# Optimization experiments

Measured on AMD Instinct MI355X. Metric: run time of the kernel, lower is better.

The kernel has to match this reference:

```python
import jax, jax.numpy as jnp
import numpy as np


def setup_inputs() -> dict:
    key = jax.random.key(0)
    k1, k2, k3 = jax.random.split(key, 3)
    N, L, S, H, D = 2, 2048, 2048, 8, 64
    return {
        "queries": jax.random.normal(k1, (N, L, H, D), dtype=jnp.float32),
        "keys": jax.random.normal(k2, (N, S, H, D), dtype=jnp.float32),
        "values": jax.random.normal(k3, (N, S, H, D), dtype=jnp.float32),
        "q_mask": jnp.ones((N, L), dtype=bool),
        "kv_mask": jnp.ones((N, S), dtype=bool),
    }


def reference(queries, keys, values, q_mask, kv_mask):
    # QK^T: [N, L, S, H]
    qk = jnp.einsum("nlhd,nshd->nlsh", queries, keys)
    # mask: True where attention is allowed
    mask = q_mask[:, :, None, None] & kv_mask[:, None, :, None]
    qk = jnp.where(mask, qk, -jnp.inf)
    softmax_temp = 1.0 / np.sqrt(queries.shape[3]).astype(np.float32)
    A = jax.nn.softmax(softmax_temp * qk, axis=2)  # over S
    out = jnp.einsum("nlsh,nshd->nlhd", A, values)
    return out
```

## Files before the change

### kernel.cpp

```cpp
#include <hip/hip_runtime.h>
#include <hip/hip_bf16.h>

#define N_B 2
#define L_Q 2048
#define S_K 2048
#define N_H 8
#define D_H 64
#define HD  512
#define KVB 64
#define NT  (S_K / KVB)
#define RS  72
#define LOG2E 1.4426950408889634f

typedef __attribute__((ext_vector_type(8))) short bf16x8;
typedef __attribute__((ext_vector_type(4))) short short4v;
typedef __attribute__((ext_vector_type(4))) float f32x4;

__device__ __forceinline__ short f2bf(float f) {
  union { float f; unsigned u; } v; v.f = f;
  return (short)((v.u + 0x7FFFu + ((v.u >> 16) & 1u)) >> 16);
}
__device__ __forceinline__ float bf2f(short s) {
  union { unsigned u; float f; } w; w.u = ((unsigned)(unsigned short)s) << 16;
  return w.f;
}
__device__ __forceinline__ bf16x8 pack8(float4 a, float4 b) {
  bf16x8 t;
  t[0]=f2bf(a.x); t[1]=f2bf(a.y); t[2]=f2bf(a.z); t[3]=f2bf(a.w);
  t[4]=f2bf(b.x); t[5]=f2bf(b.y); t[6]=f2bf(b.z); t[7]=f2bf(b.w);
  return t;
}

__global__ __launch_bounds__(256)
void preconv_kernel(const float* __restrict__ K, const float* __restrict__ V,
                    const int* __restrict__ kvm,
                    short* __restrict__ kws, short* __restrict__ vws,
                    unsigned long long* __restrict__ mws) {
  const size_t i = (size_t)blockIdx.x * 256 + threadIdx.x;
  const float4* kp = (const float4*)K + i * 2;
  float4 a = kp[0], b = kp[1];
  *(bf16x8*)(kws + i * 8) = pack8(a, b);
  const float4* vp = (const float4*)V + i * 2;
  float4 c = vp[0], d = vp[1];
  *(bf16x8*)(vws + i * 8) = pack8(c, d);
  if (blockIdx.x == 0 && threadIdx.x < (N_B * S_K / 64)) {
    const int* src = kvm + threadIdx.x * 64;
    unsigned long long m = 0;
    #pragma unroll 8
    for (int bb = 0; bb < 64; ++bb) m |= (src[bb] ? 1ull : 0ull) << bb;
    mws[threadIdx.x] = m;
  }
}

__global__ __launch_bounds__(128, 2)
void attn_fwd_v2(const float* __restrict__ Q, const short* __restrict__ Kb,
                 const short* __restrict__ Vb,
                 const unsigned long long* __restrict__ mbits,
                 float* __restrict__ Out) {
  __shared__ __align__(128) short kt[2 * 4096];
  __shared__ __align__(128) short vt[2 * 4096];
  __shared__ __align__(16)  short pl[2][16 * RS];

  const int tid  = threadIdx.x;
  const int wid  = tid >> 6;
  const int lane = tid & 63;
  const int l16  = lane & 15;
  const int lg   = lane >> 4;

  const int logical = ((blockIdx.x & 7) << 7) | (blockIdx.x >> 3);
  const int nh = logical >> 6;
  const int qb = logical & 63;
  const int n  = nh >> 3;
  const int h  = nh & 7;
  const int q0 = qb * 32 + wid * 16;

  const float* Qn = Q  + ((size_t)n * L_Q) * HD + h * D_H;
  const char*  Kn = (const char*)(Kb + ((size_t)n * S_K) * HD + h * D_H);
  const char*  Vn = (const char*)(Vb + ((size_t)n * S_K) * HD + h * D_H);

  int koffb[4], voffb[4];
  #pragma unroll
  for (int i = 0; i < 4; ++i) {
    const int p   = wid * 4096 + i * 1024 + lane * 16;
    const int row = p >> 7;
    const int cb  = (p & 127) ^ ((row & 7) << 4);
    koffb[i] = row * 1024 + cb;
    const int k  = ((p >> 9) << 2) | ((p >> 5) & 3);
    const int d  = (((p >> 7) & 3) << 4) | ((p >> 1) & 15);
    voffb[i] = k * 1024 + d * 2;
  }

  bf16x8 qf[2];
  {
    const float* qp = Qn + (size_t)(q0 + l16) * HD + lg * 8;
    #pragma unroll
    for (int c = 0; c < 2; ++c) {
      float4 a = *(const float4*)(qp + c * 32);
      float4 b = *(const float4*)(qp + c * 32 + 4);
      float4 as, bs;
      as.x=a.x*0.125f; as.y=a.y*0.125f; as.z=a.z*0.125f; as.w=a.w*0.125f;
      bs.x=b.x*0.125f; bs.y=b.y*0.125f; bs.z=b.z*0.125f; bs.w=b.w*0.125f;
      qf[c] = pack8(as, bs);
    }
  }

  const int swz    = (l16 & 7) << 4;
  const int kaddrA = l16 * 128 + ((lg * 16) ^ swz);
  const int kaddrB = l16 * 128 + ((64 + lg * 16) ^ swz);
  const int vlane  = lg * 1024 + l16 * 8;
  const unsigned kt0 = (unsigned)(size_t)(__attribute__((address_space(3))) char*)((char*)&kt[0]);
  const unsigned vt0 = (unsigned)(size_t)(__attribute__((address_space(3))) char*)((char*)&vt[0]);

  f32x4 o[4];
  #pragma unroll
  for (int g = 0; g < 4; ++g) o[g] = (f32x4){0.f, 0.f, 0.f, 0.f};
  float m_run[4], l_run[4];
  #pragma unroll
  for (int r = 0; r < 4; ++r) { m_run[r] = -3e38f; l_run[r] = 0.f; }

  short* pw = pl[wid];

  #define ISSUE(t_) do {                                                          \
    const int bs_ = ((t_) & 1) * 8192;                                            \
    const char* ks_ = Kn + (size_t)(t_) * 65536;                                  \
    const char* vs_ = Vn + (size_t)(t_) * 65536;                                  \
    _Pragma("unroll")                                                             \
    for (int i_ = 0; i_ < 4; ++i_) {                                              \
      __builtin_amdgcn_global_load_lds(                                           \
        (const __attribute__((address_space(1))) void*)(ks_ + koffb[i_]),         \
        (__attribute__((address_space(3))) void*)((char*)kt + bs_ + wid*4096 + i_*1024), \
        16, 0, 0);                                                                \
      __builtin_amdgcn_global_load_lds(                                           \
        (const __attribute__((address_space(1))) void*)(vs_ + voffb[i_]),         \
        (__attribute__((address_space(3))) void*)((char*)vt + bs_ + wid*4096 + i_*1024), \
        16, 0, 0);                                                                \
    }                                                                             \
  } while (0)

  ISSUE(0);

  for (int t = 0; t < NT; ++t) {
    __syncthreads();
    if (t + 1 < NT) ISSUE(t + 1);
    const int bo = (t & 1) * 8192;

    f32x4 sc[4];
    #pragma unroll
    for (int g = 0; g < 4; ++g) {
      bf16x8 kb0 = *(const bf16x8*)((const char*)kt + bo + g * 2048 + kaddrA);
      bf16x8 kb1 = *(const bf16x8*)((const char*)kt + bo + g * 2048 + kaddrB);
      f32x4 z = (f32x4){0.f, 0.f, 0.f, 0.f};
      z = __builtin_amdgcn_mfma_f32_16x16x32_bf16(qf[0], kb0, z, 0, 0, 0);
      z = __builtin_amdgcn_mfma_f32_16x16x32_bf16(qf[1], kb1, z, 0, 0, 0);
      sc[g] = z;
    }

    const unsigned long long mb = mbits[n * NT + t];
    #pragma unroll
    for (int g = 0; g < 4; ++g) {
      if (!((mb >> (g * 16 + l16)) & 1ull)) {
        #pragma unroll
        for (int r = 0; r < 4; ++r) sc[g][r] = -3e38f;
      }
    }

    float mt[4];
    #pragma unroll
    for (int r = 0; r < 4; ++r) {
      float v = fmaxf(fmaxf(sc[0][r], sc[1][r]), fmaxf(sc[2][r], sc[3][r]));
      v = fmaxf(v, __shfl_xor(v, 1));
      v = fmaxf(v, __shfl_xor(v, 2));
      v = fmaxf(v, __shfl_xor(v, 4));
      v = fmaxf(v, __shfl_xor(v, 8));
      mt[r] = v;
    }
    float alpha[4];
    #pragma unroll
    for (int r = 0; r < 4; ++r) {
      float mn = fmaxf(m_run[r], mt[r]);
      alpha[r] = __builtin_amdgcn_exp2f((m_run[r] - mn) * LOG2E);
      m_run[r] = mn;
    }
    float rsum[4] = {0.f, 0.f, 0.f, 0.f};
    short pb[4][4];
    #pragma unroll
    for (int g = 0; g < 4; ++g) {
      #pragma unroll
      for (int r = 0; r < 4; ++r) {
        float p = __builtin_amdgcn_exp2f((sc[g][r] - m_run[r]) * LOG2E);
        short s = f2bf(p);
        pb[g][r] = s;
        rsum[r] += bf2f(s);
      }
    }
    #pragma unroll
    for (int r = 0; r < 4; ++r) {
      float v = rsum[r];
      v += __shfl_xor(v, 1);
      v += __shfl_xor(v, 2);
      v += __shfl_xor(v, 4);
      v += __shfl_xor(v, 8);
      l_run[r] = l_run[r] * alpha[r] + v;
    }
    #pragma unroll
    for (int g = 0; g < 4; ++g) {
      f32x4 tv = o[g];
      #pragma unroll
      for (int r = 0; r < 4; ++r) tv[r] *= alpha[r];
      o[g] = tv;
    }

    #pragma unroll
    for (int g = 0; g < 4; ++g)
      #pragma unroll
      for (int r = 0; r < 4; ++r)
        pw[(lg * 4 + r) * RS + g * 16 + l16] = pb[g][r];

    bf16x8 pa0 = *(const bf16x8*)&pw[l16 * RS + lg * 8];
    bf16x8 pa1 = *(const bf16x8*)&pw[l16 * RS + 32 + lg * 8];

    const unsigned va = vt0 + (unsigned)(bo + vlane);
    #define TRRD(dst, off) asm volatile("ds_read_b64_tr_b16 %0, %1 offset:" off \
                                        : "=v"(dst) : "v"(va))
    short4v w0la, w0lb, w0ha, w0hb, w1la, w1lb, w1ha, w1hb;
    short4v w2la, w2lb, w2ha, w2hb, w3la, w3lb, w3ha, w3hb;
    TRRD(w0la, "0");   TRRD(w0lb, "512"); TRRD(w0ha, "4096"); TRRD(w0hb, "4608");
    TRRD(w1la, "128"); TRRD(w1lb, "640"); TRRD(w1ha, "4224"); TRRD(w1hb, "4736");
    TRRD(w2la, "256"); TRRD(w2lb, "768"); TRRD(w2ha, "4352"); TRRD(w2hb, "4864");
    TRRD(w3la, "384"); TRRD(w3lb, "896"); TRRD(w3ha, "4480"); TRRD(w3hb, "4992");
    asm volatile("s_waitcnt lgkmcnt(0)" ::: "memory");
    __builtin_amdgcn_sched_barrier(0);

    bf16x8 v0l = __builtin_shufflevector(w0la, w0lb, 0,1,2,3,4,5,6,7);
    bf16x8 v0h = __builtin_shufflevector(w0ha, w0hb, 0,1,2,3,4,5,6,7);
    bf16x8 v1l = __builtin_shufflevector(w1la, w1lb, 0,1,2,3,4,5,6,7);
    bf16x8 v1h = __builtin_shufflevector(w1ha, w1hb, 0,1,2,3,4,5,6,7);
    bf16x8 v2l = __builtin_shufflevector(w2la, w2lb, 0,1,2,3,4,5,6,7);
    bf16x8 v2h = __builtin_shufflevector(w2ha, w2hb, 0,1,2,3,4,5,6,7);
    bf16x8 v3l = __builtin_shufflevector(w3la, w3lb, 0,1,2,3,4,5,6,7);
    bf16x8 v3h = __builtin_shufflevector(w3ha, w3hb, 0,1,2,3,4,5,6,7);

    o[0] = __builtin_amdgcn_mfma_f32_16x16x32_bf16(pa0, v0l, o[0], 0, 0, 0);
    o[0] = __builtin_amdgcn_mfma_f32_16x16x32_bf16(pa1, v0h, o[0], 0, 0, 0);
    o[1] = __builtin_amdgcn_mfma_f32_16x16x32_bf16(pa0, v1l, o[1], 0, 0, 0);
    o[1] = __builtin_amdgcn_mfma_f32_16x16x32_bf16(pa1, v1h, o[1], 0, 0, 0);
    o[2] = __builtin_amdgcn_mfma_f32_16x16x32_bf16(pa0, v2l, o[2], 0, 0, 0);
    o[2] = __builtin_amdgcn_mfma_f32_16x16x32_bf16(pa1, v2h, o[2], 0, 0, 0);
    o[3] = __builtin_amdgcn_mfma_f32_16x16x32_bf16(pa0, v3l, o[3], 0, 0, 0);
    o[3] = __builtin_amdgcn_mfma_f32_16x16x32_bf16(pa1, v3h, o[3], 0, 0, 0);
  }

  float* op = Out + ((size_t)n * L_Q + q0) * HD + h * D_H;
  float inv[4];
  #pragma unroll
  for (int r = 0; r < 4; ++r) inv[r] = 1.0f / l_run[r];
  #pragma unroll
  for (int gd = 0; gd < 4; ++gd)
    #pragma unroll
    for (int r = 0; r < 4; ++r)
      op[(size_t)(lg * 4 + r) * HD + gd * 16 + l16] = o[gd][r] * inv[r];
}

__global__ __launch_bounds__(256, 2)
void attn_fwd_kernel(const float* __restrict__ Q, const float* __restrict__ K,
                     const float* __restrict__ V,
                     const int* __restrict__ q_mask,
                     const int* __restrict__ kv_mask,
                     float* __restrict__ Out) {
  __shared__ __align__(16) short kts[KVB * RS];
  __shared__ __align__(16) short vts[D_H * RS];
  __shared__ __align__(16) short pls[4][16 * RS];
  const int tid = threadIdx.x, wid = tid >> 6, lane = tid & 63;
  const int l16 = lane & 15, lg = lane >> 4;
  const int bid = blockIdx.x, nh = bid >> 5, qb = bid & 31;
  const int n = nh >> 3, h = nh & 7, q0 = qb * 64 + wid * 16;
  const float* Qb = Q + ((size_t)n * L_Q) * HD + h * D_H;
  const float* Kb = K + ((size_t)n * S_K) * HD + h * D_H;
  const float* Vb = V + ((size_t)n * S_K) * HD + h * D_H;
  const int* km = kv_mask + (size_t)n * S_K;
  (void)q_mask;
  bf16x8 qf[2];
  {
    const float* qp = Qb + (size_t)(q0 + l16) * HD + lg * 8;
    #pragma unroll
    for (int c = 0; c < 2; ++c) {
      float4 a = *(const float4*)(qp + c * 32);
      float4 b = *(const float4*)(qp + c * 32 + 4);
      float4 as, bs;
      as.x=a.x*0.125f; as.y=a.y*0.125f; as.z=a.z*0.125f; as.w=a.w*0.125f;
      bs.x=b.x*0.125f; bs.y=b.y*0.125f; bs.z=b.z*0.125f; bs.w=b.w*0.125f;
      qf[c] = pack8(as, bs);
    }
  }
  f32x4 o[4];
  #pragma unroll
  for (int g = 0; g < 4; ++g) o[g] = (f32x4){0.f, 0.f, 0.f, 0.f};
  float m_run[4], l_run[4];
  #pragma unroll
  for (int r = 0; r < 4; ++r) { m_run[r] = -3e38f; l_run[r] = 0.f; }
  for (int s0 = 0; s0 < S_K; s0 += KVB) {
    __syncthreads();
    {
      const int cid = tid << 1, row = cid >> 3, c0 = cid & 7;
      const float* kp = Kb + (size_t)(s0 + row) * HD + c0 * 8;
      float4 f0 = *(const float4*)(kp), f1 = *(const float4*)(kp + 4);
      float4 f2 = *(const float4*)(kp + 8), f3 = *(const float4*)(kp + 12);
      *(bf16x8*)&kts[row * RS + c0 * 8]     = pack8(f0, f1);
      *(bf16x8*)&kts[row * RS + c0 * 8 + 8] = pack8(f2, f3);
    }
    {
      const int kv = tid >> 2, dc = tid & 3;
      const float* vp = Vb + (size_t)(s0 + kv) * HD + dc * 16;
      float4 f0 = *(const float4*)(vp), f1 = *(const float4*)(vp + 4);
      float4 f2 = *(const float4*)(vp + 8), f3 = *(const float4*)(vp + 12);
      float tv[16] = { f0.x,f0.y,f0.z,f0.w, f1.x,f1.y,f1.z,f1.w,
                       f2.x,f2.y,f2.z,f2.w, f3.x,f3.y,f3.z,f3.w };
      short* dst = &vts[(dc * 16) * RS + kv];
      #pragma unroll
      for (int j = 0; j < 16; ++j) dst[j * RS] = f2bf(tv[j]);
    }
    __syncthreads();
    f32x4 sc[4];
    #pragma unroll
    for (int g = 0; g < 4; ++g) {
      bf16x8 kb0 = *(const bf16x8*)&kts[(g*16 + l16) * RS + lg * 8];
      bf16x8 kb1 = *(const bf16x8*)&kts[(g*16 + l16) * RS + 32 + lg * 8];
      f32x4 z = (f32x4){0.f, 0.f, 0.f, 0.f};
      z = __builtin_amdgcn_mfma_f32_16x16x32_bf16(qf[0], kb0, z, 0, 0, 0);
      z = __builtin_amdgcn_mfma_f32_16x16x32_bf16(qf[1], kb1, z, 0, 0, 0);
      sc[g] = z;
    }
    #pragma unroll
    for (int g = 0; g < 4; ++g) {
      float b = km[s0 + g*16 + l16] ? 0.f : -3e38f;
      #pragma unroll
      for (int r = 0; r < 4; ++r) sc[g][r] += b;
    }
    float mt[4];
    #pragma unroll
    for (int r = 0; r < 4; ++r) {
      float v = fmaxf(fmaxf(sc[0][r], sc[1][r]), fmaxf(sc[2][r], sc[3][r]));
      v = fmaxf(v, __shfl_xor(v, 1)); v = fmaxf(v, __shfl_xor(v, 2));
      v = fmaxf(v, __shfl_xor(v, 4)); v = fmaxf(v, __shfl_xor(v, 8));
      mt[r] = v;
    }
    float alpha[4];
    #pragma unroll
    for (int r = 0; r < 4; ++r) {
      float mn = fmaxf(m_run[r], mt[r]);
      alpha[r] = __builtin_amdgcn_exp2f((m_run[r] - mn) * LOG2E);
      m_run[r] = mn;
    }
    float rsum[4] = {0.f, 0.f, 0.f, 0.f};
    short pb[4][4];
    #pragma unroll
    for (int g = 0; g < 4; ++g)
      #pragma unroll
      for (int r = 0; r < 4; ++r) {
        float p = __builtin_amdgcn_exp2f((sc[g][r] - m_run[r]) * LOG2E);
        short s = f2bf(p); pb[g][r] = s; rsum[r] += bf2f(s);
      }
    #pragma unroll
    for (int r = 0; r < 4; ++r) {
      float v = rsum[r];
      v += __shfl_xor(v, 1); v += __shfl_xor(v, 2);
      v += __shfl_xor(v, 4); v += __shfl_xor(v, 8);
      l_run[r] = l_run[r] * alpha[r] + v;
    }
    #pragma unroll
    for (int g = 0; g < 4; ++g)
      #pragma unroll
      for (int r = 0; r < 4; ++r) o[g][r] *= alpha[r];
    short* pwf = pls[wid];
    #pragma unroll
    for (int g = 0; g < 4; ++g)
      #pragma unroll
      for (int r = 0; r < 4; ++r)
        pwf[(lg*4 + r) * RS + g*16 + l16] = pb[g][r];
    __syncthreads();
    bf16x8 pa0 = *(const bf16x8*)&pwf[l16 * RS + lg * 8];
    bf16x8 pa1 = *(const bf16x8*)&pwf[l16 * RS + 32 + lg * 8];
    #pragma unroll
    for (int gd = 0; gd < 4; ++gd) {
      bf16x8 vb0 = *(const bf16x8*)&vts[(gd*16 + l16) * RS + lg * 8];
      bf16x8 vb1 = *(const bf16x8*)&vts[(gd*16 + l16) * RS + 32 + lg * 8];
      o[gd] = __builtin_amdgcn_mfma_f32_16x16x32_bf16(pa0, vb0, o[gd], 0, 0, 0);
      o[gd] = __builtin_amdgcn_mfma_f32_16x16x32_bf16(pa1, vb1, o[gd], 0, 0, 0);
    }
  }
  float* op = Out + ((size_t)n * L_Q + q0) * HD + h * D_H;
  float inv[4];
  #pragma unroll
  for (int r = 0; r < 4; ++r) inv[r] = 1.0f / l_run[r];
  #pragma unroll
  for (int gd = 0; gd < 4; ++gd)
    #pragma unroll
    for (int r = 0; r < 4; ++r)
      op[(size_t)(lg*4 + r) * HD + gd*16 + l16] = o[gd][r] * inv[r];
}

extern "C" void kernel_launch(void* const* d_in, const int* in_sizes, int n_in,
                              void* d_out, int out_size, void* d_ws, size_t ws_size,
                              hipStream_t stream) {
  const float* Q = (const float*)d_in[0];
  const float* K = (const float*)d_in[1];
  const float* V = (const float*)d_in[2];
  const int* qm = (const int*)d_in[3];
  const int* km = (const int*)d_in[4];
  float* Out = (float*)d_out;
  (void)in_sizes; (void)n_in; (void)out_size;

  const size_t kbytes = (size_t)N_B * S_K * HD * 2;
  const size_t need = 2 * kbytes + 512;
  if (ws_size >= need) {
    short* kws = (short*)d_ws;
    short* vws = (short*)((char*)d_ws + kbytes);
    unsigned long long* mws = (unsigned long long*)((char*)d_ws + 2 * kbytes);
    hipLaunchKernelGGL(preconv_kernel, dim3(1024), dim3(256), 0, stream,
                       K, V, km, kws, vws, mws);
    hipLaunchKernelGGL(attn_fwd_v2, dim3(1024), dim3(128), 0, stream,
                       Q, kws, vws, mws, Out);
  } else {
    hipLaunchKernelGGL(attn_fwd_kernel, dim3(512), dim3(256), 0, stream,
                       Q, K, V, qm, km, Out);
  }
}
```

Baseline: 147.0 us.

## Rewrite attention with 32x32 MFMA, split-KV, transposed V, and lazy rescale

```diff
diff --git a/kernel.cpp b/kernel.cpp
--- a/kernel.cpp
+++ b/kernel.cpp
@@ -8,13 +8,18 @@
 #define D_H 64
 #define HD  512
 #define KVB 64
-#define NT  (S_K / KVB)
+#define NT  32
+#define NSP 3
 #define RS  72
+#define PQT ((size_t)N_B * L_Q * N_H)
 #define LOG2E 1.4426950408889634f
-
-typedef __attribute__((ext_vector_type(8))) short bf16x8;
-typedef __attribute__((ext_vector_type(4))) short short4v;
-typedef __attribute__((ext_vector_type(4))) float f32x4;
+#define DEFER_THR 11.5f
+
+typedef __attribute__((ext_vector_type(8)))  short bf16x8;
+typedef __attribute__((ext_vector_type(4)))  short short4v;
+typedef __attribute__((ext_vector_type(4)))  float f32x4;
+typedef __attribute__((ext_vector_type(16))) float f32x16;
+typedef __attribute__((ext_vector_type(4)))  unsigned int u32x4;
 
 __device__ __forceinline__ short f2bf(float f) {
   union { float f; unsigned u; } v; v.f = f;
@@ -30,19 +35,35 @@
   t[4]=f2bf(b.x); t[5]=f2bf(b.y); t[6]=f2bf(b.z); t[7]=f2bf(b.w);
   return t;
 }
+__device__ __forceinline__ unsigned cvtpk(float a, float b) {
+  unsigned d;
+  asm("v_cvt_pk_bf16_f32 %0, %1, %2" : "=v"(d) : "v"(a), "v"(b));
+  return d;
+}
 
 __global__ __launch_bounds__(256)
 void preconv_kernel(const float* __restrict__ K, const float* __restrict__ V,
                     const int* __restrict__ kvm,
-                    short* __restrict__ kws, short* __restrict__ vws,
+                    short* __restrict__ kws, short* __restrict__ vtws,
                     unsigned long long* __restrict__ mws) {
   const size_t i = (size_t)blockIdx.x * 256 + threadIdx.x;
   const float4* kp = (const float4*)K + i * 2;
   float4 a = kp[0], b = kp[1];
   *(bf16x8*)(kws + i * 8) = pack8(a, b);
-  const float4* vp = (const float4*)V + i * 2;
-  float4 c = vp[0], d = vp[1];
-  *(bf16x8*)(vws + i * 8) = pack8(c, d);
+  {
+    const size_t e0 = i * 8;
+    const float4* vp = (const float4*)(V + e0);
+    float4 c = vp[0], d = vp[1];
+    const int n   = (int)(e0 >> 20);
+    const int rem = (int)(e0 & 1048575u);
+    const int kv  = rem >> 9;
+    const int hd  = rem & 511;
+    const int h   = hd >> 6, d0 = hd & 63;
+    short* dst = vtws + ((size_t)((n * 8 + h) * 64 + d0)) * 2048 + kv;
+    float tv[8] = { c.x,c.y,c.z,c.w, d.x,d.y,d.z,d.w };
+    #pragma unroll
+    for (int j = 0; j < 8; ++j) dst[(size_t)j * 2048] = f2bf(tv[j]);
+  }
   if (blockIdx.x == 0 && threadIdx.x < (N_B * S_K / 64)) {
     const int* src = kvm + threadIdx.x * 64;
     unsigned long long m = 0;
@@ -52,213 +73,198 @@
   }
 }
 
-__global__ __launch_bounds__(128, 2)
-void attn_fwd_v2(const float* __restrict__ Q, const short* __restrict__ Kb,
-                 const short* __restrict__ Vb,
-                 const unsigned long long* __restrict__ mbits,
-                 float* __restrict__ Out) {
+__global__ __launch_bounds__(256, 3)
+void attn_fwd32(const float* __restrict__ Q, const short* __restrict__ Kb,
+                const short* __restrict__ Vtb,
+                const unsigned long long* __restrict__ mbits,
+                short* __restrict__ Owb, float* __restrict__ Mw,
+                float* __restrict__ Lw) {
   __shared__ __align__(128) short kt[2 * 4096];
   __shared__ __align__(128) short vt[2 * 4096];
-  __shared__ __align__(16)  short pl[2][16 * RS];
 
   const int tid  = threadIdx.x;
   const int wid  = tid >> 6;
   const int lane = tid & 63;
-  const int l16  = lane & 15;
-  const int lg   = lane >> 4;
-
-  const int logical = ((blockIdx.x & 7) << 7) | (blockIdx.x >> 3);
-  const int nh = logical >> 6;
-  const int qb = logical & 63;
-  const int n  = nh >> 3;
-  const int h  = nh & 7;
-  const int q0 = qb * 32 + wid * 16;
-
-  const float* Qn = Q  + ((size_t)n * L_Q) * HD + h * D_H;
-  const char*  Kn = (const char*)(Kb + ((size_t)n * S_K) * HD + h * D_H);
-  const char*  Vn = (const char*)(Vb + ((size_t)n * S_K) * HD + h * D_H);
-
-  int koffb[4], voffb[4];
-  #pragma unroll
-  for (int i = 0; i < 4; ++i) {
-    const int p   = wid * 4096 + i * 1024 + lane * 16;
+  const int l31  = lane & 31;
+  const int hi   = lane >> 5;
+
+  const int logical = (blockIdx.x & 7) * 96 + (blockIdx.x >> 3);
+  const int qb   = logical & 15;
+  const int rest = logical >> 4;
+  const int sp   = rest % NSP;
+  const int nh   = rest / NSP;
+  const int n = nh >> 3;
+  const int h = nh & 7;
+  const int q0 = qb * 128 + wid * 32;
+  const int t0 = sp * 11;
+  const int t1 = (sp == 2) ? NT : (t0 + 11);
+
+  const float* Qn  = Q + ((size_t)n * L_Q) * HD + h * D_H;
+  const char*  Kn  = (const char*)(Kb + ((size_t)n * S_K) * HD + h * D_H);
+  const char*  Vtn = (const char*)(Vtb + ((size_t)(n * 8 + h) * 64) * 2048);
+
+  int koffb[2], voffb[2];
+  #pragma unroll
+  for (int i = 0; i < 2; ++i) {
+    const int p   = tid * 16 + i * 4096;
     const int row = p >> 7;
-    const int cb  = (p & 127) ^ ((row & 7) << 4);
-    koffb[i] = row * 1024 + cb;
-    const int k  = ((p >> 9) << 2) | ((p >> 5) & 3);
-    const int d  = (((p >> 7) & 3) << 4) | ((p >> 1) & 15);
-    voffb[i] = k * 1024 + d * 2;
-  }
-
-  bf16x8 qf[2];
+    const int g   = (p & 127) ^ ((row & 7) << 4);
+    koffb[i] = row * 1024 + g;
+    voffb[i] = row * 4096 + g;
+  }
+
+  bf16x8 qf[4];
   {
-    const float* qp = Qn + (size_t)(q0 + l16) * HD + lg * 8;
-    #pragma unroll
-    for (int c = 0; c < 2; ++c) {
-      float4 a = *(const float4*)(qp + c * 32);
-      float4 b = *(const float4*)(qp + c * 32 + 4);
+    const float sq = 0.125f * LOG2E;
+    const float* qp = Qn + (size_t)(q0 + l31) * HD + hi * 8;
+    #pragma unroll
+    for (int dc = 0; dc < 4; ++dc) {
+      float4 a = *(const float4*)(qp + dc * 16);
+      float4 b = *(const float4*)(qp + dc * 16 + 4);
       float4 as, bs;
-      as.x=a.x*0.125f; as.y=a.y*0.125f; as.z=a.z*0.125f; as.w=a.w*0.125f;
-      bs.x=b.x*0.125f; bs.y=b.y*0.125f; bs.z=b.z*0.125f; bs.w=b.w*0.125f;
-      qf[c] = pack8(as, bs);
-    }
-  }
-
-  const int swz    = (l16 & 7) << 4;
-  const int kaddrA = l16 * 128 + ((lg * 16) ^ swz);
-  const int kaddrB = l16 * 128 + ((64 + lg * 16) ^ swz);
-  const int vlane  = lg * 1024 + l16 * 8;
-  const unsigned kt0 = (unsigned)(size_t)(__attribute__((address_space(3))) char*)((char*)&kt[0]);
-  const unsigned vt0 = (unsigned)(size_t)(__attribute__((address_space(3))) char*)((char*)&vt[0]);
-
-  f32x4 o[4];
-  #pragma unroll
-  for (int g = 0; g < 4; ++g) o[g] = (f32x4){0.f, 0.f, 0.f, 0.f};
-  float m_run[4], l_run[4];
-  #pragma unroll
-  for (int r = 0; r < 4; ++r) { m_run[r] = -3e38f; l_run[r] = 0.f; }
-
-  short* pw = pl[wid];
+      as.x=a.x*sq; as.y=a.y*sq; as.z=a.z*sq; as.w=a.w*sq;
+      bs.x=b.x*sq; bs.y=b.y*sq; bs.z=b.z*sq; bs.w=b.w*sq;
+      qf[dc] = pack8(as, bs);
+    }
+  }
+
+  const int swz = (l31 & 7) << 4;
+  f32x16 o0 = {}, o1 = {};
+  float m = 0.f, ls = 0.f;
 
   #define ISSUE(t_) do {                                                          \
     const int bs_ = ((t_) & 1) * 8192;                                            \
     const char* ks_ = Kn + (size_t)(t_) * 65536;                                  \
-    const char* vs_ = Vn + (size_t)(t_) * 65536;                                  \
+    const char* vs_ = Vtn + (size_t)(t_) * 128;                                   \
     _Pragma("unroll")                                                             \
-    for (int i_ = 0; i_ < 4; ++i_) {                                              \
+    for (int i_ = 0; i_ < 2; ++i_) {                                              \
       __builtin_amdgcn_global_load_lds(                                           \
         (const __attribute__((address_space(1))) void*)(ks_ + koffb[i_]),         \
-        (__attribute__((address_space(3))) void*)((char*)kt + bs_ + wid*4096 + i_*1024), \
+        (__attribute__((address_space(3))) void*)((char*)kt + bs_ + wid*1024 + i_*4096), \
         16, 0, 0);                                                                \
       __builtin_amdgcn_global_load_lds(                                           \
         (const __attribute__((address_space(1))) void*)(vs_ + voffb[i_]),         \
-        (__attribute__((address_space(3))) void*)((char*)vt + bs_ + wid*4096 + i_*1024), \
+        (__attribute__((address_space(3))) void*)((char*)vt + bs_ + wid*1024 + i_*4096), \
         16, 0, 0);                                                                \
     }                                                                             \
   } while (0)
 
-  ISSUE(0);
-
-  for (int t = 0; t < NT; ++t) {
+  ISSUE(t0);
+
+  for (int t = t0; t < t1; ++t) {
     __syncthreads();
-    if (t + 1 < NT) ISSUE(t + 1);
+    if (t + 1 < t1) ISSUE(t + 1);
     const int bo = (t & 1) * 8192;
 
-    f32x4 sc[4];
-    #pragma unroll
-    for (int g = 0; g < 4; ++g) {
-      bf16x8 kb0 = *(const bf16x8*)((const char*)kt + bo + g * 2048 + kaddrA);
-      bf16x8 kb1 = *(const bf16x8*)((const char*)kt + bo + g * 2048 + kaddrB);
-      f32x4 z = (f32x4){0.f, 0.f, 0.f, 0.f};
-      z = __builtin_amdgcn_mfma_f32_16x16x32_bf16(qf[0], kb0, z, 0, 0, 0);
-      z = __builtin_amdgcn_mfma_f32_16x16x32_bf16(qf[1], kb1, z, 0, 0, 0);
-      sc[g] = z;
+    f32x16 a0 = {}, a1 = {};
+    #pragma unroll
+    for (int dc = 0; dc < 4; ++dc) {
+      const int co = (dc * 32 + hi * 16) ^ swz;
+      bf16x8 kf0 = *(const bf16x8*)((const char*)kt + bo + l31 * 128 + co);
+      bf16x8 kf1 = *(const bf16x8*)((const char*)kt + bo + (32 + l31) * 128 + co);
+      a0 = __builtin_amdgcn_mfma_f32_32x32x16_bf16(kf0, qf[dc], a0, 0, 0, 0);
+      a1 = __builtin_amdgcn_mfma_f32_32x32x16_bf16(kf1, qf[dc], a1, 0, 0, 0);
     }
 
     const unsigned long long mb = mbits[n * NT + t];
-    #pragma unroll
-    for (int g = 0; g < 4; ++g) {
-      if (!((mb >> (g * 16 + l16)) & 1ull)) {
-        #pragma unroll
-        for (int r = 0; r < 4; ++r) sc[g][r] = -3e38f;
+    if (mb != ~0ull) {
+      #pragma unroll
+      for (int r = 0; r < 16; ++r) {
+        const int kv0 = (r & 3) + 8 * (r >> 2) + 4 * hi;
+        if (!((mb >> kv0) & 1ull))        a0[r] = -3e38f;
+        if (!((mb >> (kv0 + 32)) & 1ull)) a1[r] = -3e38f;
       }
     }
 
-    float mt[4];
-    #pragma unroll
-    for (int r = 0; r < 4; ++r) {
-      float v = fmaxf(fmaxf(sc[0][r], sc[1][r]), fmaxf(sc[2][r], sc[3][r]));
-      v = fmaxf(v, __shfl_xor(v, 1));
-      v = fmaxf(v, __shfl_xor(v, 2));
-      v = fmaxf(v, __shfl_xor(v, 4));
-      v = fmaxf(v, __shfl_xor(v, 8));
-      mt[r] = v;
-    }
-    float alpha[4];
-    #pragma unroll
-    for (int r = 0; r < 4; ++r) {
-      float mn = fmaxf(m_run[r], mt[r]);
-      alpha[r] = __builtin_amdgcn_exp2f((m_run[r] - mn) * LOG2E);
-      m_run[r] = mn;
-    }
-    float rsum[4] = {0.f, 0.f, 0.f, 0.f};
-    short pb[4][4];
-    #pragma unroll
-    for (int g = 0; g < 4; ++g) {
-      #pragma unroll
-      for (int r = 0; r < 4; ++r) {
-        float p = __builtin_amdgcn_exp2f((sc[g][r] - m_run[r]) * LOG2E);
-        short s = f2bf(p);
-        pb[g][r] = s;
-        rsum[r] += bf2f(s);
-      }
-    }
-    #pragma unroll
-    for (int r = 0; r < 4; ++r) {
-      float v = rsum[r];
-      v += __shfl_xor(v, 1);
-      v += __shfl_xor(v, 2);
-      v += __shfl_xor(v, 4);
-      v += __shfl_xor(v, 8);
-      l_run[r] = l_run[r] * alpha[r] + v;
-    }
-    #pragma unroll
-    for (int g = 0; g < 4; ++g) {
-      f32x4 tv = o[g];
-      #pragma unroll
-      for (int r = 0; r < 4; ++r) tv[r] *= alpha[r];
-      o[g] = tv;
-    }
-
-    #pragma unroll
-    for (int g = 0; g < 4; ++g)
-      #pragma unroll
-      for (int r = 0; r < 4; ++r)
-        pw[(lg * 4 + r) * RS + g * 16 + l16] = pb[g][r];
-
-    bf16x8 pa0 = *(const bf16x8*)&pw[l16 * RS + lg * 8];
-    bf16x8 pa1 = *(const bf16x8*)&pw[l16 * RS + 32 + lg * 8];
-
-    const unsigned va = vt0 + (unsigned)(bo + vlane);
-    #define TRRD(dst, off) asm volatile("ds_read_b64_tr_b16 %0, %1 offset:" off \
-                                        : "=v"(dst) : "v"(va))
-    short4v w0la, w0lb, w0ha, w0hb, w1la, w1lb, w1ha, w1hb;
-    short4v w2la, w2lb, w2ha, w2hb, w3la, w3lb, w3ha, w3hb;
-    TRRD(w0la, "0");   TRRD(w0lb, "512"); TRRD(w0ha, "4096"); TRRD(w0hb, "4608");
-    TRRD(w1la, "128"); TRRD(w1lb, "640"); TRRD(w1ha, "4224"); TRRD(w1hb, "4736");
-    TRRD(w2la, "256"); TRRD(w2lb, "768"); TRRD(w2ha, "4352"); TRRD(w2hb, "4864");
-    TRRD(w3la, "384"); TRRD(w3lb, "896"); TRRD(w3ha, "4480"); TRRD(w3hb, "4992");
-    asm volatile("s_waitcnt lgkmcnt(0)" ::: "memory");
-    __builtin_amdgcn_sched_barrier(0);
-
-    bf16x8 v0l = __builtin_shufflevector(w0la, w0lb, 0,1,2,3,4,5,6,7);
-    bf16x8 v0h = __builtin_shufflevector(w0ha, w0hb, 0,1,2,3,4,5,6,7);
-    bf16x8 v1l = __builtin_shufflevector(w1la, w1lb, 0,1,2,3,4,5,6,7);
-    bf16x8 v1h = __builtin_shufflevector(w1ha, w1hb, 0,1,2,3,4,5,6,7);
-    bf16x8 v2l = __builtin_shufflevector(w2la, w2lb, 0,1,2,3,4,5,6,7);
-    bf16x8 v2h = __builtin_shufflevector(w2ha, w2hb, 0,1,2,3,4,5,6,7);
-    bf16x8 v3l = __builtin_shufflevector(w3la, w3lb, 0,1,2,3,4,5,6,7);
-    bf16x8 v3h = __builtin_shufflevector(w3ha, w3hb, 0,1,2,3,4,5,6,7);
-
-    o[0] = __builtin_amdgcn_mfma_f32_16x16x32_bf16(pa0, v0l, o[0], 0, 0, 0);
-    o[0] = __builtin_amdgcn_mfma_f32_16x16x32_bf16(pa1, v0h, o[0], 0, 0, 0);
-    o[1] = __builtin_amdgcn_mfma_f32_16x16x32_bf16(pa0, v1l, o[1], 0, 0, 0);
-    o[1] = __builtin_amdgcn_mfma_f32_16x16x32_bf16(pa1, v1h, o[1], 0, 0, 0);
-    o[2] = __builtin_amdgcn_mfma_f32_16x16x32_bf16(pa0, v2l, o[2], 0, 0, 0);
-    o[2] = __builtin_amdgcn_mfma_f32_16x16x32_bf16(pa1, v2h, o[2], 0, 0, 0);
-    o[3] = __builtin_amdgcn_mfma_f32_16x16x32_bf16(pa0, v3l, o[3], 0, 0, 0);
-    o[3] = __builtin_amdgcn_mfma_f32_16x16x32_bf16(pa1, v3h, o[3], 0, 0, 0);
-  }
-
-  float* op = Out + ((size_t)n * L_Q + q0) * HD + h * D_H;
-  float inv[4];
-  #pragma unroll
-  for (int r = 0; r < 4; ++r) inv[r] = 1.0f / l_run[r];
-  #pragma unroll
-  for (int gd = 0; gd < 4; ++gd)
-    #pragma unroll
-    for (int r = 0; r < 4; ++r)
-      op[(size_t)(lg * 4 + r) * HD + gd * 16 + l16] = o[gd][r] * inv[r];
+    float pm = a0[0];
+    #pragma unroll
+    for (int r = 1; r < 16; ++r) pm = fmaxf(pm, a0[r]);
+    #pragma unroll
+    for (int r = 0; r < 16; ++r) pm = fmaxf(pm, a1[r]);
+    if (!__all(pm <= m + DEFER_THR)) {
+      float mx = fmaxf(pm, __shfl_xor(pm, 32));
+      float mn = fmaxf(m, mx);
+      float al = __builtin_amdgcn_exp2f(m - mn);
+      m = mn;
+      #pragma unroll
+      for (int r = 0; r < 16; ++r) { o0[r] *= al; o1[r] *= al; }
+      ls *= al;
+    }
+
+    float psum = 0.f;
+    #pragma unroll
+    for (int r = 0; r < 16; ++r) {
+      a0[r] = __builtin_amdgcn_exp2f(a0[r] - m); psum += a0[r];
+      a1[r] = __builtin_amdgcn_exp2f(a1[r] - m); psum += a1[r];
+    }
+    ls += psum;
+
+    u32x4 paw[4];
+    #pragma unroll
+    for (int ks = 0; ks < 4; ++ks) {
+      const int ro = (ks & 1) * 8;
+      float e0, e1, e2, e3, e4, e5, e6, e7;
+      if (ks < 2) { e0=a0[ro]; e1=a0[ro+1]; e2=a0[ro+2]; e3=a0[ro+3];
+                    e4=a0[ro+4]; e5=a0[ro+5]; e6=a0[ro+6]; e7=a0[ro+7]; }
+      else        { e0=a1[ro]; e1=a1[ro+1]; e2=a1[ro+2]; e3=a1[ro+3];
+                    e4=a1[ro+4]; e5=a1[ro+5]; e6=a1[ro+6]; e7=a1[ro+7]; }
+      unsigned x = cvtpk(e0, e1), y = cvtpk(e2, e3);
+      unsigned u = cvtpk(e4, e5), v = cvtpk(e6, e7);
+      unsigned xs = __shfl_xor(x, 32), ys = __shfl_xor(y, 32);
+      unsigned us = __shfl_xor(u, 32), vs = __shfl_xor(v, 32);
+      u32x4 w;
+      w[0] = hi ? us : x;  w[1] = hi ? vs : y;
+      w[2] = hi ? u  : xs; w[3] = hi ? v  : ys;
+      paw[ks] = w;
+    }
+
+    #pragma unroll
+    for (int ks = 0; ks < 4; ++ks) {
+      const bf16x8 pa = *(const bf16x8*)&paw[ks];
+      const int co = (ks * 32 + hi * 16) ^ swz;
+      bf16x8 vf0 = *(const bf16x8*)((const char*)vt + bo + l31 * 128 + co);
+      bf16x8 vf1 = *(const bf16x8*)((const char*)vt + bo + (32 + l31) * 128 + co);
+      o0 = __builtin_amdgcn_mfma_f32_32x32x16_bf16(pa, vf0, o0, 0, 0, 0);
+      o1 = __builtin_amdgcn_mfma_f32_32x32x16_bf16(pa, vf1, o1, 0, 0, 0);
+    }
+  }
+
+  const float lst = ls + __shfl_xor(ls, 32);
+  #pragma unroll
+  for (int r = 0; r < 16; ++r) {
+    const int qrow = q0 + ((r & 3) + 8 * (r >> 2) + 4 * hi);
+    const size_t rowidx = ((size_t)n * L_Q + qrow) * N_H + h;
+    const size_t ob = ((size_t)sp * PQT + rowidx) * D_H;
+    Owb[ob + l31]      = f2bf(o0[r]);
+    Owb[ob + 32 + l31] = f2bf(o1[r]);
+  }
+  if (lane < 32) {
+    const int qrow = q0 + lane;
+    const size_t rowidx = ((size_t)n * L_Q + qrow) * N_H + h;
+    Mw[(size_t)sp * PQT + rowidx] = m;
+    Lw[(size_t)sp * PQT + rowidx] = lst;
+  }
+}
+
+__global__ __launch_bounds__(256)
+void combine_kernel(const short* __restrict__ Owb, const float* __restrict__ Mw,
+                    const float* __restrict__ Lw, float* __restrict__ Out) {
+  const int gid = blockIdx.x * 256 + threadIdx.x;
+  const size_t rid = (size_t)(gid >> 4);
+  const int d0 = (gid & 15) << 2;
+  float M = fmaxf(fmaxf(Mw[rid], Mw[PQT + rid]), Mw[2 * PQT + rid]);
+  float lsum = 0.f, ax = 0.f, ay = 0.f, az = 0.f, aw = 0.f;
+  #pragma unroll
+  for (int j = 0; j < NSP; ++j) {
+    const float w = __builtin_amdgcn_exp2f(Mw[j * PQT + rid] - M);
+    lsum += Lw[j * PQT + rid] * w;
+    const short4v ov = *(const short4v*)(Owb + (j * PQT + rid) * D_H + d0);
+    ax += bf2f(ov[0]) * w; ay += bf2f(ov[1]) * w;
+    az += bf2f(ov[2]) * w; aw += bf2f(ov[3]) * w;
+  }
+  const float inv = 1.0f / lsum;
+  float4 r; r.x = ax * inv; r.y = ay * inv; r.z = az * inv; r.w = aw * inv;
+  *(float4*)(Out + rid * D_H + d0) = r;
 }
 
 __global__ __launch_bounds__(256, 2)
@@ -410,16 +416,25 @@
   float* Out = (float*)d_out;
   (void)in_sizes; (void)n_in; (void)out_size;
 
-  const size_t kbytes = (size_t)N_B * S_K * HD * 2;
-  const size_t need = 2 * kbytes + 512;
+  const size_t kbytes  = (size_t)N_B * S_K * HD * 2;
+  const size_t base_ml = 2 * kbytes + 1024;
+  const size_t mlb     = (size_t)NSP * PQT * sizeof(float);
+  const size_t owbb    = (size_t)NSP * PQT * D_H * 2;
+  const size_t need    = base_ml + 2 * mlb + owbb;
+
   if (ws_size >= need) {
-    short* kws = (short*)d_ws;
-    short* vws = (short*)((char*)d_ws + kbytes);
+    short* kws  = (short*)d_ws;
+    short* vtws = (short*)((char*)d_ws + kbytes);
     unsigned long long* mws = (unsigned long long*)((char*)d_ws + 2 * kbytes);
+    float* Mw  = (float*)((char*)d_ws + base_ml);
+    float* Lw  = Mw + NSP * PQT;
+    short* Owb = (short*)(Lw + NSP * PQT);
     hipLaunchKernelGGL(preconv_kernel, dim3(1024), dim3(256), 0, stream,
-                       K, V, km, kws, vws, mws);
-    hipLaunchKernelGGL(attn_fwd_v2, dim3(1024), dim3(128), 0, stream,
-                       Q, kws, vws, mws, Out);
+                       K, V, km, kws, vtws, mws);
+    hipLaunchKernelGGL(attn_fwd32, dim3(768), dim3(256), 0, stream,
+                       Q, kws, vtws, mws, Owb, Mw, Lw);
+    hipLaunchKernelGGL(combine_kernel, dim3(2048), dim3(256), 0, stream,
+                       Owb, Mw, Lw, Out);
   } else {
     hipLaunchKernelGGL(attn_fwd_kernel, dim3(512), dim3(256), 0, stream,
                        Q, K, V, qm, km, Out);
```

Measured after the change: 122.1 us. 17.0% less time.
